# Kernel tuning notes

Measured on AMD Instinct MI355X. Metric: run time of the kernel, lower is better.

## Reference

```python
import jax, jax.numpy as jnp
import numpy as np

M_CH = 2        # channels == sources
K = 8           # NMF bases
N_ITER = 8
SWITCH_ITER = 5
ALPHA = 0.1
BETA = 0.0
EPS = 1e-10
I_BINS = 1025   # freq bins (n_fft=2048)
J_FRAMES = 4096 # STFT frames


def setup_inputs() -> dict:
    key = jax.random.key(0)
    ks = jax.random.split(key, 5)
    X = jax.random.normal(ks[0], (M_CH, J_FRAMES, I_BINS, 2), jnp.float32)
    T_s = jax.random.uniform(ks[1], (I_BINS, K), jnp.float32) * 0.1 + EPS
    V_s = jax.random.uniform(ks[2], (K, J_FRAMES), jnp.float32) * 0.1 + EPS
    T_n = jax.random.uniform(ks[3], (I_BINS, K), jnp.float32) * 0.1 + EPS
    V_n = jax.random.uniform(ks[4], (K, J_FRAMES), jnp.float32) * 0.1 + EPS
    return {"X": X, "T_s": T_s, "V_s": V_s, "T_n": T_n, "V_n": V_n}


def _ilrma_noisy(X, T_s, V_s, T_n, V_n):
    M, J, I, _ = X.shape
    eps, alpha, beta = EPS, ALPHA, BETA
    # (M,J,I,2) -> complex (I,M,J)
    Xc = (X[..., 0] + 1j * X[..., 1]).astype(jnp.complex64).transpose(2, 0, 1)
    eyeM = jnp.eye(M, dtype=jnp.complex64)
    W = jnp.broadcast_to(eyeM, (I, M, M))
    Y = jnp.einsum('inm,inj->imj', W.conj(), Xc)  # W^H X
    lam_n = jnp.ones((I,), jnp.float32)
    r_s = jnp.maximum(T_s @ V_s, eps)
    r_n = jnp.maximum(T_n @ V_n, eps)

    for it in range(N_ITER):
        if it < SWITCH_ITER:
            r_s = jnp.maximum(T_s @ V_s, eps)
            r_n = jnp.maximum(T_n @ V_n, eps)
        lam = lam_n[:, None]
        Lam = jnp.maximum(r_s + r_n * lam, eps)
        Y1 = Y[:, 0, :]
        p1 = jnp.abs(Y1) ** 2                          # (I,J)
        pn = jnp.sum(jnp.abs(Y[:, 1:, :]) ** 2, axis=1)  # (I,J)
        invL = 1.0 / Lam
        invL2 = invL * invL
        if it < SWITCH_ITER:
            # --- T_s ---
            T_s = jnp.maximum(T_s * jnp.sqrt(((p1 * invL2) @ V_s.T) / ((invL @ V_s.T) + eps)), eps)
            r_s = jnp.maximum(T_s @ V_s, eps)
            Lam = jnp.maximum(r_s + r_n * lam, eps); invL = 1.0 / Lam; invL2 = invL * invL
            # --- V_s ---
            V_s = jnp.maximum(V_s * jnp.sqrt((T_s.T @ (p1 * invL2)) / ((T_s.T @ invL) + eps)), eps)
            r_s = jnp.maximum(T_s @ V_s, eps)
            Lam = jnp.maximum(r_s + r_n * lam, eps); invL = 1.0 / Lam; invL2 = invL * invL
            inv_rn = 1.0 / r_n; inv_rn2 = inv_rn * inv_rn
            # --- T_n ---
            Tn_num = (lam * p1 * invL2) @ V_n.T + (pn * inv_rn2) @ V_n.T
            Tn_den = (lam * invL) @ V_n.T + (M - 1) * (inv_rn @ V_n.T) + eps
            T_n = jnp.maximum(T_n * jnp.sqrt(Tn_num / Tn_den), eps)
            r_n = jnp.maximum(T_n @ V_n, eps)
            Lam = jnp.maximum(r_s + r_n * lam, eps); invL = 1.0 / Lam; invL2 = invL * invL
            inv_rn = 1.0 / r_n; inv_rn2 = inv_rn * inv_rn
            # --- V_n ---
            Vn_num = T_n.T @ (lam * p1 * invL2) + T_n.T @ (pn * inv_rn2)
            Vn_den = T_n.T @ (lam * invL) + (M - 1) * (T_n.T @ inv_rn) + eps
            V_n = jnp.maximum(V_n * jnp.sqrt(Vn_num / Vn_den), eps)
            r_n = jnp.maximum(T_n @ V_n, eps)
            r_s = jnp.maximum(T_s @ V_s, eps)
            Lam = jnp.maximum(r_s + r_n * lam, eps); invL = 1.0 / Lam; invL2 = invL * invL
            # --- lambda_n ---
            lam_num = jnp.sum(r_n * p1 * invL2, axis=1)
            lam_den = jnp.sum(r_n * invL, axis=1) + eps
            lam_n = jnp.maximum(lam_n * jnp.sqrt(lam_num / lam_den), eps)
            Lam = jnp.maximum(r_s + r_n * lam_n[:, None], eps)
            # --- GEVD demixing update per frequency bin ---
            Xw_s = Xc * jnp.sqrt(1.0 / Lam)[:, None, :]
            Xw_n = Xc * jnp.sqrt(1.0 / r_n)[:, None, :]
            G_s = jnp.einsum('imj,inj->imn', Xw_s, Xw_s.conj()) / J + eps * eyeM
            G_n = jnp.einsum('imj,inj->imn', Xw_n, Xw_n.conj()) / J + eps * eyeM
            L = jnp.linalg.cholesky(G_s)
            Linv = jnp.linalg.inv(L)
            LinvH = jnp.conj(jnp.swapaxes(Linv, 1, 2))
            C = Linv @ G_n @ LinvH
            evals, evecs = jnp.linalg.eigh(C)  # ascending eigenvalues
            Vg = LinvH @ evecs                 # (I,M,M) generalized eigenvectors
            cols = []
            for m in range(M):
                h = Vg[:, :, m]                # (I,M); eigh already sorts ascending
                G = G_s if m == 0 else G_n
                quad = jnp.real(jnp.einsum('im,imn,in->i', h.conj(), G, h))
                cols.append(h / jnp.sqrt(jnp.maximum(quad, eps))[:, None])
            W = jnp.stack(cols, axis=2)
            Y = jnp.einsum('inm,inj->imj', W.conj(), Xc)
        else:
            # Phase 2: fix W, unconstrained r updates with inverse-gamma prior
            inv_rs = 1.0 / (r_s + eps); inv_rs2 = inv_rs * inv_rs
            inv_rn = 1.0 / (r_n + eps); inv_rn2 = inv_rn * inv_rn
            r_s = jnp.maximum(r_s * jnp.sqrt((p1 * invL2 + beta * inv_rs2) / (invL + (alpha + 1.0) * inv_rs + eps)), eps)
            Lam = jnp.maximum(r_s + r_n * lam, eps); invL = 1.0 / Lam; invL2 = invL * invL
            r_n = jnp.maximum(r_n * jnp.sqrt((lam * p1 * invL2 + pn * inv_rn2) / (lam * invL + (M - 1) * inv_rn + eps)), eps)
            Lam = jnp.maximum(r_s + r_n * lam, eps); invL = 1.0 / Lam; invL2 = invL * invL
            lam_num = jnp.sum(r_n * p1 * invL2, axis=1)
            lam_den = jnp.sum(r_n * invL, axis=1) + eps
            lam_n = jnp.maximum(lam_n * jnp.sqrt(lam_num / lam_den), eps)

    # Final single-channel Wiener extraction of the target, replicated over M
    Lam = jnp.maximum(r_s + r_n * lam_n[:, None], eps)
    S = (r_s / Lam) * Y[:, 0, :]                       # (I,J) complex
    S_ri = jnp.stack([jnp.real(S).T, jnp.imag(S).T], axis=-1)  # (J,I,2)
    return jnp.broadcast_to(S_ri[None], (M, J, I, 2)).astype(jnp.float32)


def reference(X, T_s, V_s, T_n, V_n):
    return _ilrma_noisy(X, T_s, V_s, T_n, V_n)
```

## Files before the change

kernel.cpp:

```cpp
#include <hip/hip_runtime.h>
#include <math.h>

#define IB 1025
#define JF 4096
#define EPSF 1e-10f

__device__ __forceinline__ void load8(const float* __restrict__ base, int i, float v[8]) {
  const float4* b4 = (const float4*)(base + i * 8);
  float4 a = b4[0], b = b4[1];
  v[0]=a.x; v[1]=a.y; v[2]=a.z; v[3]=a.w; v[4]=b.x; v[5]=b.y; v[6]=b.z; v[7]=b.w;
}
__device__ __forceinline__ float dot8(const float a[8], const float b[8]) {
  float s = a[0]*b[0];
#pragma unroll
  for (int k=1;k<8;k++) s += a[k]*b[k];
  return s;
}

__global__ __launch_bounds__(256) void k_init(
    const float* __restrict__ Ts_in, const float* __restrict__ Vs_in,
    const float* __restrict__ Tn_in, const float* __restrict__ Vn_in,
    float* __restrict__ Ts, float* __restrict__ Vs,
    float* __restrict__ Tn, float* __restrict__ Vn,
    float* __restrict__ lam, float* __restrict__ Wm) {
  int idx = blockIdx.x * 256 + threadIdx.x;
  if (idx < 8 * JF) { Vs[idx] = Vs_in[idx]; Vn[idx] = Vn_in[idx]; }
  if (idx < IB * 8) { Ts[idx] = Ts_in[idx]; Tn[idx] = Tn_in[idx]; }
  if (idx < IB) {
    lam[idx] = 1.0f;
    float* w = Wm + idx * 8;
    w[0]=1.f; w[1]=0.f; w[2]=0.f; w[3]=0.f; w[4]=0.f; w[5]=0.f; w[6]=1.f; w[7]=0.f;
  }
}

__global__ __launch_bounds__(1024) void k_p1pn_ts(const float2* __restrict__ X2,
    const float* __restrict__ Wm,
    const float* __restrict__ Ts, const float* __restrict__ Vs,
    const float* __restrict__ Tn, const float* __restrict__ Vn,
    const float* __restrict__ lam,
    float* __restrict__ p1, float* __restrict__ pn, float* __restrict__ P) {
  int tx = threadIdx.x, ty = threadIdx.y;
  int i = blockIdx.x * 256 + tx;
  int jc = blockIdx.y;
  bool ok = (i < IB);
  float ts[8], tn[8], lamv = 0.f;
  float4 wa = make_float4(0,0,0,0), wb = make_float4(0,0,0,0);
  if (ok) {
    load8(Ts, i, ts); load8(Tn, i, tn); lamv = lam[i];
    const float4* W4 = (const float4*)Wm;
    wa = W4[i*2]; wb = W4[i*2+1];
  }
  float num[8] = {0,0,0,0,0,0,0,0}, den[8] = {0,0,0,0,0,0,0,0};
  int j0 = jc * 16 + ty * 4;
  for (int jj = 0; jj < 4; jj++) {
    int j = j0 + jj;
    float vs[8], vn[8];
#pragma unroll
    for (int k=0;k<8;k++){ vs[k]=Vs[k*JF+j]; vn[k]=Vn[k*JF+j]; }
    if (ok) {
      float2 x0 = X2[j*IB + i];
      float2 x1 = X2[(JF + j)*IB + i];
      float y0r = wa.x*x0.x + wa.y*x0.y + wa.z*x1.x + wa.w*x1.y;
      float y0i = wa.x*x0.y - wa.y*x0.x + wa.z*x1.y - wa.w*x1.x;
      float y1r = wb.x*x0.x + wb.y*x0.y + wb.z*x1.x + wb.w*x1.y;
      float y1i = wb.x*x0.y - wb.y*x0.x + wb.z*x1.y - wb.w*x1.x;
      float pv  = y0r*y0r + y0i*y0i;
      float pnv = y1r*y1r + y1i*y1i;
      p1[j*IB + i] = pv;
      pn[j*IB + i] = pnv;
      float rs = fmaxf(dot8(ts, vs), EPSF);
      float rn = fmaxf(dot8(tn, vn), EPSF);
      float iL = 1.f / fmaxf(rs + rn*lamv, EPSF);
      float a2 = pv*iL*iL;
#pragma unroll
      for (int k=0;k<8;k++){ num[k] += a2*vs[k]; den[k] += iL*vs[k]; }
    }
  }
  __shared__ float red[16][4][256];
#pragma unroll
  for (int v=0;v<8;v++){ red[v][ty][tx] = num[v]; red[8+v][ty][tx] = den[v]; }
  __syncthreads();
  if (ok) {
#pragma unroll
    for (int u=0;u<4;u++){
      int v = ty*4+u;
      float s = red[v][0][tx]+red[v][1][tx]+red[v][2][tx]+red[v][3][tx];
      P[(jc*16+v)*IB + i] = s;
    }
  }
}

__global__ __launch_bounds__(512) void k_t_final(const float* __restrict__ P, float* __restrict__ T) {
  int tx = threadIdx.x;
  int ii = tx & 63, g = tx >> 6;
  int i = blockIdx.x * 64 + ii;
  int k = blockIdx.y;
  float num = 0.f, den = 0.f;
  if (i < IB) {
    for (int t = 0; t < 32; t++) {
      int c = g*32 + t;
      num += P[(c*16+k)*IB + i];
      den += P[(c*16+8+k)*IB + i];
    }
  }
  __shared__ float red[2][8][64];
  red[0][g][ii] = num; red[1][g][ii] = den;
  __syncthreads();
  if (g == 0 && i < IB) {
    float n_ = 0.f, d_ = 0.f;
#pragma unroll
    for (int q=0;q<8;q++){ n_ += red[0][q][ii]; d_ += red[1][q][ii]; }
    float t = T[i*8+k];
    T[i*8+k] = fmaxf(t * sqrtf(n_/(d_+EPSF)), EPSF);
  }
}

__global__ __launch_bounds__(256) void k_vs(const float* __restrict__ p1,
    const float* __restrict__ Ts, float* __restrict__ Vs,
    const float* __restrict__ Tn, const float* __restrict__ Vn,
    const float* __restrict__ lam) {
  int j = blockIdx.x;
  int tx = threadIdx.x;
  float vs[8], vn[8];
#pragma unroll
  for (int k=0;k<8;k++){ vs[k]=Vs[k*JF+j]; vn[k]=Vn[k*JF+j]; }
  float acc[16];
#pragma unroll
  for (int v=0;v<16;v++) acc[v] = 0.f;
  for (int s = 0; s < 5; s++) {
    int i = s*256 + tx;
    if (i < IB) {
      float ts[8], tn[8];
      load8(Ts, i, ts); load8(Tn, i, tn);
      float lamv = lam[i];
      float pv = p1[j*IB + i];
      float rs = fmaxf(dot8(ts, vs), EPSF);
      float rn = fmaxf(dot8(tn, vn), EPSF);
      float iL = 1.f / fmaxf(rs + rn*lamv, EPSF);
      float a2 = pv*iL*iL;
#pragma unroll
      for (int k=0;k<8;k++){ acc[k] += ts[k]*a2; acc[8+k] += ts[k]*iL; }
    }
  }
  __shared__ float red[4][16];
  int wid = tx >> 6, lane = tx & 63;
#pragma unroll
  for (int v=0;v<16;v++){
    float x = acc[v];
    x += __shfl_down(x, 32, 64); x += __shfl_down(x, 16, 64);
    x += __shfl_down(x, 8, 64);  x += __shfl_down(x, 4, 64);
    x += __shfl_down(x, 2, 64);  x += __shfl_down(x, 1, 64);
    if (lane == 0) red[wid][v] = x;
  }
  __syncthreads();
  if (tx == 0) {
#pragma unroll
    for (int k=0;k<8;k++){
      float n_ = red[0][k]+red[1][k]+red[2][k]+red[3][k];
      float d_ = red[0][8+k]+red[1][8+k]+red[2][8+k]+red[3][8+k];
      Vs[k*JF+j] = fmaxf(vs[k] * sqrtf(n_/(d_+EPSF)), EPSF);
    }
  }
}

__global__ __launch_bounds__(1024) void k_tn_partial(const float* __restrict__ p1,
    const float* __restrict__ pn,
    const float* __restrict__ Ts, const float* __restrict__ Vs,
    const float* __restrict__ Tn, const float* __restrict__ Vn,
    const float* __restrict__ lam, float* __restrict__ P) {
  int tx = threadIdx.x, ty = threadIdx.y;
  int i = blockIdx.x * 256 + tx;
  int jc = blockIdx.y;
  bool ok = (i < IB);
  float ts[8], tn[8], lamv = 0.f;
  if (ok) { load8(Ts, i, ts); load8(Tn, i, tn); lamv = lam[i]; }
  float num[8] = {0,0,0,0,0,0,0,0}, den[8] = {0,0,0,0,0,0,0,0};
  int j0 = jc * 16 + ty * 4;
  for (int jj = 0; jj < 4; jj++) {
    int j = j0 + jj;
    float vs[8], vn[8];
#pragma unroll
    for (int k=0;k<8;k++){ vs[k]=Vs[k*JF+j]; vn[k]=Vn[k*JF+j]; }
    if (ok) {
      float pv = p1[j*IB + i];
      float pnv = pn[j*IB + i];
      float rs = fmaxf(dot8(ts, vs), EPSF);
      float rn = fmaxf(dot8(tn, vn), EPSF);
      float iL = 1.f / fmaxf(rs + rn*lamv, EPSF);
      float irn = 1.f / rn;
      float a2 = lamv*pv*iL*iL + pnv*irn*irn;
      float b2 = lamv*iL + irn;
#pragma unroll
      for (int k=0;k<8;k++){ num[k] += a2*vn[k]; den[k] += b2*vn[k]; }
    }
  }
  __shared__ float red[16][4][256];
#pragma unroll
  for (int v=0;v<8;v++){ red[v][ty][tx] = num[v]; red[8+v][ty][tx] = den[v]; }
  __syncthreads();
  if (ok) {
#pragma unroll
    for (int u=0;u<4;u++){
      int v = ty*4+u;
      float s = red[v][0][tx]+red[v][1][tx]+red[v][2][tx]+red[v][3][tx];
      P[(jc*16+v)*IB + i] = s;
    }
  }
}

__global__ __launch_bounds__(256) void k_vn(const float* __restrict__ p1,
    const float* __restrict__ pn,
    const float* __restrict__ Ts, const float* __restrict__ Vs,
    const float* __restrict__ Tn, float* __restrict__ Vn,
    const float* __restrict__ lam) {
  int j = blockIdx.x;
  int tx = threadIdx.x;
  float vs[8], vn[8];
#pragma unroll
  for (int k=0;k<8;k++){ vs[k]=Vs[k*JF+j]; vn[k]=Vn[k*JF+j]; }
  float acc[16];
#pragma unroll
  for (int v=0;v<16;v++) acc[v] = 0.f;
  for (int s = 0; s < 5; s++) {
    int i = s*256 + tx;
    if (i < IB) {
      float ts[8], tn[8];
      load8(Ts, i, ts); load8(Tn, i, tn);
      float lamv = lam[i];
      float pv = p1[j*IB + i];
      float pnv = pn[j*IB + i];
      float rs = fmaxf(dot8(ts, vs), EPSF);
      float rn = fmaxf(dot8(tn, vn), EPSF);
      float iL = 1.f / fmaxf(rs + rn*lamv, EPSF);
      float irn = 1.f / rn;
      float a2 = lamv*pv*iL*iL + pnv*irn*irn;
      float b2 = lamv*iL + irn;
#pragma unroll
      for (int k=0;k<8;k++){ acc[k] += tn[k]*a2; acc[8+k] += tn[k]*b2; }
    }
  }
  __shared__ float red[4][16];
  int wid = tx >> 6, lane = tx & 63;
#pragma unroll
  for (int v=0;v<16;v++){
    float x = acc[v];
    x += __shfl_down(x, 32, 64); x += __shfl_down(x, 16, 64);
    x += __shfl_down(x, 8, 64);  x += __shfl_down(x, 4, 64);
    x += __shfl_down(x, 2, 64);  x += __shfl_down(x, 1, 64);
    if (lane == 0) red[wid][v] = x;
  }
  __syncthreads();
  if (tx == 0) {
#pragma unroll
    for (int k=0;k<8;k++){
      float n_ = red[0][k]+red[1][k]+red[2][k]+red[3][k];
      float d_ = red[0][8+k]+red[1][8+k]+red[2][8+k]+red[3][8+k];
      Vn[k*JF+j] = fmaxf(vn[k] * sqrtf(n_/(d_+EPSF)), EPSF);
    }
  }
}

__global__ __launch_bounds__(1024) void k_lam_partial(const float* __restrict__ p1,
    const float* __restrict__ Ts, const float* __restrict__ Vs,
    const float* __restrict__ Tn, const float* __restrict__ Vn,
    const float* __restrict__ lam, float* __restrict__ P) {
  int tx = threadIdx.x, ty = threadIdx.y;
  int i = blockIdx.x * 256 + tx;
  int jc = blockIdx.y;
  bool ok = (i < IB);
  float ts[8], tn[8], lamv = 0.f;
  if (ok) { load8(Ts, i, ts); load8(Tn, i, tn); lamv = lam[i]; }
  float lnum = 0.f, lden = 0.f;
  int j0 = jc * 16 + ty * 4;
  for (int jj = 0; jj < 4; jj++) {
    int j = j0 + jj;
    float vs[8], vn[8];
#pragma unroll
    for (int k=0;k<8;k++){ vs[k]=Vs[k*JF+j]; vn[k]=Vn[k*JF+j]; }
    if (ok) {
      float pv = p1[j*IB + i];
      float rs = fmaxf(dot8(ts, vs), EPSF);
      float rn = fmaxf(dot8(tn, vn), EPSF);
      float iL = 1.f / fmaxf(rs + rn*lamv, EPSF);
      lnum += rn*pv*iL*iL;
      lden += rn*iL;
    }
  }
  __shared__ float red[2][4][256];
  red[0][ty][tx] = lnum; red[1][ty][tx] = lden;
  __syncthreads();
  if (ty < 2 && ok) {
    float s = red[ty][0][tx]+red[ty][1][tx]+red[ty][2][tx]+red[ty][3][tx];
    P[(jc*2+ty)*IB + i] = s;
  }
}

__global__ __launch_bounds__(512) void k_lam_final(const float* __restrict__ P, float* __restrict__ lam,
                                                   int nchunks) {
  int tx = threadIdx.x;
  int ii = tx & 63, g = tx >> 6;
  int i = blockIdx.x * 64 + ii;
  int per = nchunks >> 3;
  float num = 0.f, den = 0.f;
  if (i < IB) {
    for (int t = 0; t < per; t++) {
      int c = g*per + t;
      num += P[(c*2+0)*IB + i];
      den += P[(c*2+1)*IB + i];
    }
  }
  __shared__ float red[2][8][64];
  red[0][g][ii] = num; red[1][g][ii] = den;
  __syncthreads();
  if (g == 0 && i < IB) {
    float n_ = 0.f, d_ = 0.f;
#pragma unroll
    for (int q=0;q<8;q++){ n_ += red[0][q][ii]; d_ += red[1][q][ii]; }
    lam[i] = fmaxf(lam[i] * sqrtf(n_/(d_+EPSF)), EPSF);
  }
}

__global__ __launch_bounds__(1024) void k_g_partial(const float2* __restrict__ X2,
    const float* __restrict__ Ts, const float* __restrict__ Vs,
    const float* __restrict__ Tn, const float* __restrict__ Vn,
    const float* __restrict__ lam, float* __restrict__ P) {
  int tx = threadIdx.x, ty = threadIdx.y;
  int i = blockIdx.x * 256 + tx;
  int jc = blockIdx.y;
  bool ok = (i < IB);
  float ts[8], tn[8], lamv = 0.f;
  if (ok) { load8(Ts, i, ts); load8(Tn, i, tn); lamv = lam[i]; }
  float g[8];
#pragma unroll
  for (int v=0;v<8;v++) g[v] = 0.f;
  int j0 = jc * 16 + ty * 4;
  for (int jj = 0; jj < 4; jj++) {
    int j = j0 + jj;
    float vs[8], vn[8];
#pragma unroll
    for (int k=0;k<8;k++){ vs[k]=Vs[k*JF+j]; vn[k]=Vn[k*JF+j]; }
    if (ok) {
      float2 x0 = X2[j*IB + i];
      float2 x1 = X2[(JF + j)*IB + i];
      float rs = fmaxf(dot8(ts, vs), EPSF);
      float rn = fmaxf(dot8(tn, vn), EPSF);
      float ws = 1.f / fmaxf(rs + rn*lamv, EPSF);
      float wn = 1.f / rn;
      float m00 = x0.x*x0.x + x0.y*x0.y;
      float m11 = x1.x*x1.x + x1.y*x1.y;
      float m01r = x0.x*x1.x + x0.y*x1.y;
      float m01i = x0.y*x1.x - x0.x*x1.y;
      g[0] += m00*ws; g[1] += m11*ws; g[2] += m01r*ws; g[3] += m01i*ws;
      g[4] += m00*wn; g[5] += m11*wn; g[6] += m01r*wn; g[7] += m01i*wn;
    }
  }
  __shared__ float red[8][4][256];
#pragma unroll
  for (int v=0;v<8;v++) red[v][ty][tx] = g[v];
  __syncthreads();
  if (ok) {
#pragma unroll
    for (int u=0;u<2;u++){
      int v = ty*2+u;
      float s = red[v][0][tx]+red[v][1][tx]+red[v][2][tx]+red[v][3][tx];
      P[(jc*8+v)*IB + i] = s;
    }
  }
}

__global__ __launch_bounds__(512) void k_g_final(const float* __restrict__ P, double* __restrict__ Gd) {
  int tx = threadIdx.x;
  int ii = tx & 63, g = tx >> 6;
  int i = blockIdx.x * 64 + ii;
  int v = blockIdx.y;
  double s = 0.0;
  if (i < IB) {
    for (int t = 0; t < 32; t++) {
      int c = g*32 + t;
      s += (double)P[(c*8+v)*IB + i];
    }
  }
  __shared__ double red[8][64];
  red[g][ii] = s;
  __syncthreads();
  if (g == 0 && i < IB) {
    double acc = 0.0;
#pragma unroll
    for (int q=0;q<8;q++) acc += red[q][ii];
    Gd[v*1028 + i] = acc;
  }
}

__device__ void dlaev2_dev(double a, double b, double c,
                           double& rt1, double& rt2, double& cs1, double& sn1) {
  double sm = a + c, df = a - c;
  double adf = fabs(df);
  double tb = b + b;
  double ab = fabs(tb);
  double acmx, acmn;
  if (fabs(a) > fabs(c)) { acmx = a; acmn = c; } else { acmx = c; acmn = a; }
  double rt;
  if (adf > ab)      { double t = ab/adf; rt = adf*sqrt(1.0 + t*t); }
  else if (adf < ab) { double t = adf/ab; rt = ab*sqrt(1.0 + t*t); }
  else               rt = ab*sqrt(2.0);
  int sgn1;
  if (sm < 0.0)      { rt1 = 0.5*(sm - rt); sgn1 = -1; rt2 = (acmx/rt1)*acmn - (b/rt1)*b; }
  else if (sm > 0.0) { rt1 = 0.5*(sm + rt); sgn1 =  1; rt2 = (acmx/rt1)*acmn - (b/rt1)*b; }
  else               { rt1 = 0.5*rt; rt2 = -0.5*rt; sgn1 = 1; }
  double cs; int sgn2;
  if (df >= 0.0) { cs = df + rt; sgn2 = 1; } else { cs = df - rt; sgn2 = -1; }
  double acs = fabs(cs);
  if (acs > ab) {
    double ct = -tb/cs;
    sn1 = 1.0/sqrt(1.0 + ct*ct);
    cs1 = ct*sn1;
  } else {
    if (ab == 0.0) { cs1 = 1.0; sn1 = 0.0; }
    else { double tn = -cs/tb; cs1 = 1.0/sqrt(1.0 + tn*tn); sn1 = tn*cs1; }
  }
  if (sgn1 == sgn2) { double tn = cs1; cs1 = -sn1; sn1 = tn; }
}

__global__ __launch_bounds__(64) void k_eig(const double* __restrict__ Gd, float* __restrict__ Wm) {
  int i = blockIdx.x * 64 + threadIdx.x;
  if (i >= IB) return;
  double g[8];
#pragma unroll
  for (int v=0;v<8;v++) g[v] = Gd[v*1028 + i];
  const double EPSD = 1e-10;
  double as  = g[0]/4096.0 + EPSD;
  double cs_ = g[1]/4096.0 + EPSD;
  double bsr = g[2]/4096.0, bsi = g[3]/4096.0;
  double dn  = g[4]/4096.0 + EPSD;
  double fn  = g[5]/4096.0 + EPSD;
  double enr = g[6]/4096.0, eni = g[7]/4096.0;
  double l11 = sqrt(as);
  double il11 = 1.0/l11;
  double l21r = bsr*il11, l21i = -bsi*il11;
  double l22sq = cs_ - (l21r*l21r + l21i*l21i);
  double l22 = sqrt(fmax(l22sq, 0.0));
  double p = il11, r = 1.0/l22;
  double qr = -l21r*p*r, qi = -l21i*p*r;
  double C00  = p*p*dn;
  double C01r = p*(dn*qr + enr*r);
  double C01i = p*(-dn*qi + eni*r);
  double C11  = (qr*qr+qi*qi)*dn + 2.0*r*(qr*enr - qi*eni) + r*r*fn;
  double br = C01r, bi = C01i;
  double e_, hqr, hqi;
  if (bi == 0.0) { e_ = br; hqr = 1.0; hqi = 0.0; }
  else {
    double ab_ = sqrt(br*br + bi*bi);
    e_ = (br >= 0.0) ? -ab_ : ab_;
    hqr = br / e_; hqi = -bi / e_;
  }
  double ut0, ub0, ut1, ub1;
  const double MEPS = 1.1102230246251565e-16;
  if (fabs(e_) <= sqrt(fabs(C00))*sqrt(fabs(C11))*MEPS) {
    if (C11 < C00) { ut0=0.0; ub0=1.0; ut1=1.0; ub1=0.0; }
    else           { ut0=1.0; ub0=0.0; ut1=0.0; ub1=1.0; }
  } else {
    double rt1, rt2, cs1, sn1;
    dlaev2_dev(C00, e_, C11, rt1, rt2, cs1, sn1);
    if (rt2 < rt1) { ut0=-sn1; ub0=cs1; ut1=cs1;  ub1=sn1; }
    else           { ut0=cs1;  ub0=sn1; ut1=-sn1; ub1=cs1; }
  }
  double chr = qr*hqr + qi*hqi;
  double chi = qr*hqi - qi*hqr;
  double v0tr = p*ut0 + chr*ub0, v0ti = chi*ub0;
  double v0br = r*hqr*ub0,       v0bi = r*hqi*ub0;
  double v1tr = p*ut1 + chr*ub1, v1ti = chi*ub1;
  double v1br = r*hqr*ub1,       v1bi = r*hqi*ub1;
  double q0 = as*(v0tr*v0tr+v0ti*v0ti) + cs_*(v0br*v0br+v0bi*v0bi)
            + 2.0*((bsr*v0br - bsi*v0bi)*v0tr + (bsr*v0bi + bsi*v0br)*v0ti);
  double q1 = dn*(v1tr*v1tr+v1ti*v1ti) + fn*(v1br*v1br+v1bi*v1bi)
            + 2.0*((enr*v1br - eni*v1bi)*v1tr + (enr*v1bi + eni*v1br)*v1ti);
  double s0 = 1.0/sqrt(fmax(q0, 1e-10));
  double s1 = 1.0/sqrt(fmax(q1, 1e-10));
  float* w = Wm + i*8;
  w[0] = (float)(v0tr*s0); w[1] = (float)(v0ti*s0);
  w[2] = (float)(v0br*s0); w[3] = (float)(v0bi*s0);
  w[4] = (float)(v1tr*s1); w[5] = (float)(v1ti*s1);
  w[6] = (float)(v1br*s1); w[7] = (float)(v1bi*s1);
}

__global__ __launch_bounds__(256) void k_p1pn_rinit(const float2* __restrict__ X2,
    const float* __restrict__ Wm,
    const float* __restrict__ Ts, const float* __restrict__ Vs,
    const float* __restrict__ Tn, const float* __restrict__ Vn,
    float* __restrict__ p1, float* __restrict__ pn, float2* __restrict__ m0) {
  int i = blockIdx.x * 256 + threadIdx.x;
  int j = blockIdx.y;
  if (i >= IB) return;
  float2 x0 = X2[j*IB + i];
  float2 x1 = X2[(JF + j)*IB + i];
  const float4* W4 = (const float4*)Wm;
  float4 wa = W4[i*2], wb = W4[i*2+1];
  float y0r = wa.x*x0.x + wa.y*x0.y + wa.z*x1.x + wa.w*x1.y;
  float y0i = wa.x*x0.y - wa.y*x0.x + wa.z*x1.y - wa.w*x1.x;
  float y1r = wb.x*x0.x + wb.y*x0.y + wb.z*x1.x + wb.w*x1.y;
  float y1i = wb.x*x0.y - wb.y*x0.x + wb.z*x1.y - wb.w*x1.x;
  p1[j*IB + i] = y0r*y0r + y0i*y0i;
  pn[j*IB + i] = y1r*y1r + y1i*y1i;
  float ts[8], tn[8];
  load8(Ts, i, ts); load8(Tn, i, tn);
  float rs = 0.f, rn = 0.f;
#pragma unroll
  for (int k=0;k<8;k++){ rs += ts[k]*Vs[k*JF+j]; rn += tn[k]*Vn[k*JF+j]; }
  m0[j*IB + i] = make_float2(fmaxf(rs, EPSF), fmaxf(rn, EPSF));
}

__global__ __launch_bounds__(1024) void k_simp(float2* __restrict__ m0,
    const float* __restrict__ p1, const float* __restrict__ pn,
    const float* __restrict__ lam, float* __restrict__ P) {
  int tx = threadIdx.x, ty = threadIdx.y;
  int i = blockIdx.x * 256 + tx;
  int jc = blockIdx.y;
  bool ok = (i < IB);
  float lamv = ok ? lam[i] : 0.f;
  float lnum = 0.f, lden = 0.f;
  int j0 = jc * 32 + ty * 8;
  for (int jj = 0; jj < 8; jj++) {
    int j = j0 + jj;
    if (ok) {
      float2 rr = m0[j*IB + i];
      float rs = rr.x, rn = rr.y;
      float pv = p1[j*IB + i], pnv = pn[j*IB + i];
      float iL = 1.f / fmaxf(rs + rn*lamv, EPSF);
      float irs = 1.f / (rs + EPSF);
      float rs2 = fmaxf(rs * sqrtf((pv*iL*iL) / (iL + 1.1f*irs + EPSF)), EPSF);
      float iL2 = 1.f / fmaxf(rs2 + rn*lamv, EPSF);
      float irn = 1.f / (rn + EPSF);
      float rn2 = fmaxf(rn * sqrtf((lamv*pv*iL2*iL2 + pnv*irn*irn) / (lamv*iL2 + irn + EPSF)), EPSF);
      float iL3 = 1.f / fmaxf(rs2 + rn2*lamv, EPSF);
      m0[j*IB + i] = make_float2(rs2, rn2);
      lnum += rn2*pv*iL3*iL3;
      lden += rn2*iL3;
    }
  }
  __shared__ float red[2][4][256];
  red[0][ty][tx] = lnum; red[1][ty][tx] = lden;
  __syncthreads();
  if (ty < 2 && ok) {
    float s = red[ty][0][tx]+red[ty][1][tx]+red[ty][2][tx]+red[ty][3][tx];
    P[(jc*2+ty)*IB + i] = s;
  }
}

__global__ __launch_bounds__(256) void k_final(float2* __restrict__ m0, float2* __restrict__ m1,
    const float2* __restrict__ X2, const float* __restrict__ Wm, const float* __restrict__ lam) {
  int i = blockIdx.x * 256 + threadIdx.x;
  int j = blockIdx.y;
  if (i >= IB) return;
  float2 rr = m0[j*IB + i];
  float L = fmaxf(rr.x + rr.y*lam[i], EPSF);
  float gsc = rr.x / L;
  float2 x0 = X2[j*IB + i];
  float2 x1 = X2[(JF + j)*IB + i];
  float4 wa = ((const float4*)Wm)[i*2];
  float y0r = wa.x*x0.x + wa.y*x0.y + wa.z*x1.x + wa.w*x1.y;
  float y0i = wa.x*x0.y - wa.y*x0.x + wa.z*x1.y - wa.w*x1.x;
  float2 s = make_float2(gsc*y0r, gsc*y0i);
  m0[j*IB + i] = s;
  m1[j*IB + i] = s;
}

extern "C" void kernel_launch(void* const* d_in, const int* in_sizes, int n_in,
                              void* d_out, int out_size, void* d_ws, size_t ws_size,
                              hipStream_t stream) {
  (void)in_sizes; (void)n_in; (void)out_size; (void)ws_size;
  const float* X = (const float*)d_in[0];
  const float* Ts_in = (const float*)d_in[1];
  const float* Vs_in = (const float*)d_in[2];
  const float* Tn_in = (const float*)d_in[3];
  const float* Vn_in = (const float*)d_in[4];

  float* w = (float*)d_ws;
  float* Pt  = w;
  double* Gd = (double*)(w + 1049600);
  float* Ts  = w + 1049600 + 16448;
  float* Vs  = Ts + 8200;
  float* Tn  = Vs + 32768;
  float* Vn  = Tn + 8200;
  float* lam = Vn + 32768;
  float* Wm  = lam + 1028;

  float* out = (float*)d_out;
  float2* m0 = (float2*)d_out;
  float2* m1 = m0 + (size_t)JF*IB;
  float* p1 = out + 2*(size_t)JF*IB;
  float* pn = p1 + (size_t)JF*IB;
  float* Pbig = out;
  const float2* X2 = (const float2*)X;

  k_init<<<dim3(128), 256, 0, stream>>>(Ts_in, Vs_in, Tn_in, Vn_in, Ts, Vs, Tn, Vn, lam, Wm);

  for (int it = 0; it < 5; it++) {
    k_p1pn_ts<<<dim3(5, 256), dim3(256,4), 0, stream>>>(X2, Wm, Ts, Vs, Tn, Vn, lam, p1, pn, Pbig);
    k_t_final<<<dim3(17, 8), 512, 0, stream>>>(Pbig, Ts);
    k_vs<<<dim3(JF), 256, 0, stream>>>(p1, Ts, Vs, Tn, Vn, lam);
    k_tn_partial<<<dim3(5, 256), dim3(256,4), 0, stream>>>(p1, pn, Ts, Vs, Tn, Vn, lam, Pbig);
    k_t_final<<<dim3(17, 8), 512, 0, stream>>>(Pbig, Tn);
    k_vn<<<dim3(JF), 256, 0, stream>>>(p1, pn, Ts, Vs, Tn, Vn, lam);
    k_lam_partial<<<dim3(5, 256), dim3(256,4), 0, stream>>>(p1, Ts, Vs, Tn, Vn, lam, Pbig);
    k_lam_final<<<dim3(17), 512, 0, stream>>>(Pbig, lam, 256);
    k_g_partial<<<dim3(5, 256), dim3(256,4), 0, stream>>>(X2, Ts, Vs, Tn, Vn, lam, Pbig);
    k_g_final<<<dim3(17, 8), 512, 0, stream>>>(Pbig, Gd);
    k_eig<<<dim3(17), 64, 0, stream>>>(Gd, Wm);
  }

  k_p1pn_rinit<<<dim3(5, JF), 256, 0, stream>>>(X2, Wm, Ts, Vs, Tn, Vn, p1, pn, m0);

  for (int it = 0; it < 3; it++) {
    k_simp<<<dim3(5, 128), dim3(256,4), 0, stream>>>(m0, p1, pn, lam, Pt);
    k_lam_final<<<dim3(17), 512, 0, stream>>>(Pt, lam, 128);
  }

  k_final<<<dim3(5, JF), 256, 0, stream>>>(m0, m1, X2, Wm, lam);
}
```

Measured before the change: 1.043 ms.

## Stage V columns in shared memory and drop intra-block j reduction in partial kernels

The partial-reduction kernels now use 256-thread blocks, each thread handling 16 frames serially. The 16x8 V slices are staged once into shared memory instead of every thread re-reading them from global memory. The shared-memory cross-ty reduction and its barrier are removed, and partials are written directly. k_simp now uses 256 chunks of 16 frames to match, which doubles the partials k_lam_final has to reduce. Blocks get smaller with longer serial loops, so there are fewer waves per block and less latency hiding per thread.

```diff
diff --git a/kernel.cpp b/kernel.cpp
--- a/kernel.cpp
+++ b/kernel.cpp
@@ -11,6 +11,12 @@
   v[0]=a.x; v[1]=a.y; v[2]=a.z; v[3]=a.w; v[4]=b.x; v[5]=b.y; v[6]=b.z; v[7]=b.w;
 }
 __device__ __forceinline__ float dot8(const float a[8], const float b[8]) {
+  float s = a[0]*b[0];
+#pragma unroll
+  for (int k=1;k<8;k++) s += a[k]*b[k];
+  return s;
+}
+__device__ __forceinline__ float dot8s(const float a[8], const float* __restrict__ b) {
   float s = a[0]*b[0];
 #pragma unroll
   for (int k=1;k<8;k++) s += a[k]*b[k];
@@ -33,60 +39,58 @@
   }
 }
 
-__global__ __launch_bounds__(1024) void k_p1pn_ts(const float2* __restrict__ X2,
+#define STAGE_V(vsh, vnh, Vs, Vn, j0) do {                                  \
+    int t_ = threadIdx.x;                                                   \
+    if (t_ < 128) { int jj_ = t_ >> 3, k_ = t_ & 7;                         \
+      vsh[jj_][k_] = Vs[k_*JF + (j0) + jj_]; }                              \
+    else { int u_ = t_ - 128; int jj_ = u_ >> 3, k_ = u_ & 7;               \
+      vnh[jj_][k_] = Vn[k_*JF + (j0) + jj_]; }                              \
+    __syncthreads();                                                        \
+  } while (0)
+
+__global__ __launch_bounds__(256) void k_p1pn_ts(const float2* __restrict__ X2,
     const float* __restrict__ Wm,
     const float* __restrict__ Ts, const float* __restrict__ Vs,
     const float* __restrict__ Tn, const float* __restrict__ Vn,
     const float* __restrict__ lam,
     float* __restrict__ p1, float* __restrict__ pn, float* __restrict__ P) {
-  int tx = threadIdx.x, ty = threadIdx.y;
+  __shared__ float vsh[16][8], vnh[16][8];
+  int tx = threadIdx.x;
   int i = blockIdx.x * 256 + tx;
   int jc = blockIdx.y;
-  bool ok = (i < IB);
-  float ts[8], tn[8], lamv = 0.f;
-  float4 wa = make_float4(0,0,0,0), wb = make_float4(0,0,0,0);
-  if (ok) {
-    load8(Ts, i, ts); load8(Tn, i, tn); lamv = lam[i];
-    const float4* W4 = (const float4*)Wm;
-    wa = W4[i*2]; wb = W4[i*2+1];
-  }
+  int j0 = jc * 16;
+  STAGE_V(vsh, vnh, Vs, Vn, j0);
+  if (i >= IB) return;
+  float ts[8], tn[8];
+  load8(Ts, i, ts); load8(Tn, i, tn);
+  float lamv = lam[i];
+  const float4* W4 = (const float4*)Wm;
+  float4 wa = W4[i*2], wb = W4[i*2+1];
   float num[8] = {0,0,0,0,0,0,0,0}, den[8] = {0,0,0,0,0,0,0,0};
-  int j0 = jc * 16 + ty * 4;
-  for (int jj = 0; jj < 4; jj++) {
+#pragma unroll 4
+  for (int jj = 0; jj < 16; jj++) {
     int j = j0 + jj;
-    float vs[8], vn[8];
-#pragma unroll
-    for (int k=0;k<8;k++){ vs[k]=Vs[k*JF+j]; vn[k]=Vn[k*JF+j]; }
-    if (ok) {
-      float2 x0 = X2[j*IB + i];
-      float2 x1 = X2[(JF + j)*IB + i];
-      float y0r = wa.x*x0.x + wa.y*x0.y + wa.z*x1.x + wa.w*x1.y;
-      float y0i = wa.x*x0.y - wa.y*x0.x + wa.z*x1.y - wa.w*x1.x;
-      float y1r = wb.x*x0.x + wb.y*x0.y + wb.z*x1.x + wb.w*x1.y;
-      float y1i = wb.x*x0.y - wb.y*x0.x + wb.z*x1.y - wb.w*x1.x;
-      float pv  = y0r*y0r + y0i*y0i;
-      float pnv = y1r*y1r + y1i*y1i;
-      p1[j*IB + i] = pv;
-      pn[j*IB + i] = pnv;
-      float rs = fmaxf(dot8(ts, vs), EPSF);
-      float rn = fmaxf(dot8(tn, vn), EPSF);
-      float iL = 1.f / fmaxf(rs + rn*lamv, EPSF);
-      float a2 = pv*iL*iL;
-#pragma unroll
-      for (int k=0;k<8;k++){ num[k] += a2*vs[k]; den[k] += iL*vs[k]; }
-    }
-  }
-  __shared__ float red[16][4][256];
-#pragma unroll
-  for (int v=0;v<8;v++){ red[v][ty][tx] = num[v]; red[8+v][ty][tx] = den[v]; }
-  __syncthreads();
-  if (ok) {
-#pragma unroll
-    for (int u=0;u<4;u++){
-      int v = ty*4+u;
-      float s = red[v][0][tx]+red[v][1][tx]+red[v][2][tx]+red[v][3][tx];
-      P[(jc*16+v)*IB + i] = s;
-    }
+    float2 x0 = X2[j*IB + i];
+    float2 x1 = X2[(JF + j)*IB + i];
+    float y0r = wa.x*x0.x + wa.y*x0.y + wa.z*x1.x + wa.w*x1.y;
+    float y0i = wa.x*x0.y - wa.y*x0.x + wa.z*x1.y - wa.w*x1.x;
+    float y1r = wb.x*x0.x + wb.y*x0.y + wb.z*x1.x + wb.w*x1.y;
+    float y1i = wb.x*x0.y - wb.y*x0.x + wb.z*x1.y - wb.w*x1.x;
+    float pv  = y0r*y0r + y0i*y0i;
+    float pnv = y1r*y1r + y1i*y1i;
+    p1[j*IB + i] = pv;
+    pn[j*IB + i] = pnv;
+    float rs = fmaxf(dot8s(ts, vsh[jj]), EPSF);
+    float rn = fmaxf(dot8s(tn, vnh[jj]), EPSF);
+    float iL = 1.f / fmaxf(rs + rn*lamv, EPSF);
+    float a2 = pv*iL*iL;
+#pragma unroll
+    for (int k=0;k<8;k++){ num[k] += a2*vsh[jj][k]; den[k] += iL*vsh[jj][k]; }
+  }
+#pragma unroll
+  for (int k=0;k<8;k++){
+    P[(jc*16+k)*IB + i] = num[k];
+    P[(jc*16+8+k)*IB + i] = den[k];
   }
 }
 
@@ -163,48 +167,40 @@
   }
 }
 
-__global__ __launch_bounds__(1024) void k_tn_partial(const float* __restrict__ p1,
+__global__ __launch_bounds__(256) void k_tn_partial(const float* __restrict__ p1,
     const float* __restrict__ pn,
     const float* __restrict__ Ts, const float* __restrict__ Vs,
     const float* __restrict__ Tn, const float* __restrict__ Vn,
     const float* __restrict__ lam, float* __restrict__ P) {
-  int tx = threadIdx.x, ty = threadIdx.y;
+  __shared__ float vsh[16][8], vnh[16][8];
+  int tx = threadIdx.x;
   int i = blockIdx.x * 256 + tx;
   int jc = blockIdx.y;
-  bool ok = (i < IB);
-  float ts[8], tn[8], lamv = 0.f;
-  if (ok) { load8(Ts, i, ts); load8(Tn, i, tn); lamv = lam[i]; }
+  int j0 = jc * 16;
+  STAGE_V(vsh, vnh, Vs, Vn, j0);
+  if (i >= IB) return;
+  float ts[8], tn[8];
+  load8(Ts, i, ts); load8(Tn, i, tn);
+  float lamv = lam[i];
   float num[8] = {0,0,0,0,0,0,0,0}, den[8] = {0,0,0,0,0,0,0,0};
-  int j0 = jc * 16 + ty * 4;
-  for (int jj = 0; jj < 4; jj++) {
+#pragma unroll 4
+  for (int jj = 0; jj < 16; jj++) {
     int j = j0 + jj;
-    float vs[8], vn[8];
-#pragma unroll
-    for (int k=0;k<8;k++){ vs[k]=Vs[k*JF+j]; vn[k]=Vn[k*JF+j]; }
-    if (ok) {
-      float pv = p1[j*IB + i];
-      float pnv = pn[j*IB + i];
-      float rs = fmaxf(dot8(ts, vs), EPSF);
-      float rn = fmaxf(dot8(tn, vn), EPSF);
-      float iL = 1.f / fmaxf(rs + rn*lamv, EPSF);
-      float irn = 1.f / rn;
-      float a2 = lamv*pv*iL*iL + pnv*irn*irn;
-      float b2 = lamv*iL + irn;
-#pragma unroll
-      for (int k=0;k<8;k++){ num[k] += a2*vn[k]; den[k] += b2*vn[k]; }
-    }
-  }
-  __shared__ float red[16][4][256];
-#pragma unroll
-  for (int v=0;v<8;v++){ red[v][ty][tx] = num[v]; red[8+v][ty][tx] = den[v]; }
-  __syncthreads();
-  if (ok) {
-#pragma unroll
-    for (int u=0;u<4;u++){
-      int v = ty*4+u;
-      float s = red[v][0][tx]+red[v][1][tx]+red[v][2][tx]+red[v][3][tx];
-      P[(jc*16+v)*IB + i] = s;
-    }
+    float pv = p1[j*IB + i];
+    float pnv = pn[j*IB + i];
+    float rs = fmaxf(dot8s(ts, vsh[jj]), EPSF);
+    float rn = fmaxf(dot8s(tn, vnh[jj]), EPSF);
+    float iL = 1.f / fmaxf(rs + rn*lamv, EPSF);
+    float irn = 1.f / rn;
+    float a2 = lamv*pv*iL*iL + pnv*irn*irn;
+    float b2 = lamv*iL + irn;
+#pragma unroll
+    for (int k=0;k<8;k++){ num[k] += a2*vnh[jj][k]; den[k] += b2*vnh[jj][k]; }
+  }
+#pragma unroll
+  for (int k=0;k<8;k++){
+    P[(jc*16+k)*IB + i] = num[k];
+    P[(jc*16+8+k)*IB + i] = den[k];
   }
 }
 
@@ -260,39 +256,33 @@
   }
 }
 
-__global__ __launch_bounds__(1024) void k_lam_partial(const float* __restrict__ p1,
+__global__ __launch_bounds__(256) void k_lam_partial(const float* __restrict__ p1,
     const float* __restrict__ Ts, const float* __restrict__ Vs,
     const float* __restrict__ Tn, const float* __restrict__ Vn,
     const float* __restrict__ lam, float* __restrict__ P) {
-  int tx = threadIdx.x, ty = threadIdx.y;
+  __shared__ float vsh[16][8], vnh[16][8];
+  int tx = threadIdx.x;
   int i = blockIdx.x * 256 + tx;
   int jc = blockIdx.y;
-  bool ok = (i < IB);
-  float ts[8], tn[8], lamv = 0.f;
-  if (ok) { load8(Ts, i, ts); load8(Tn, i, tn); lamv = lam[i]; }
+  int j0 = jc * 16;
+  STAGE_V(vsh, vnh, Vs, Vn, j0);
+  if (i >= IB) return;
+  float ts[8], tn[8];
+  load8(Ts, i, ts); load8(Tn, i, tn);
+  float lamv = lam[i];
   float lnum = 0.f, lden = 0.f;
-  int j0 = jc * 16 + ty * 4;
-  for (int jj = 0; jj < 4; jj++) {
+#pragma unroll 4
+  for (int jj = 0; jj < 16; jj++) {
     int j = j0 + jj;
-    float vs[8], vn[8];
-#pragma unroll
-    for (int k=0;k<8;k++){ vs[k]=Vs[k*JF+j]; vn[k]=Vn[k*JF+j]; }
-    if (ok) {
-      float pv = p1[j*IB + i];
-      float rs = fmaxf(dot8(ts, vs), EPSF);
-      float rn = fmaxf(dot8(tn, vn), EPSF);
-      float iL = 1.f / fmaxf(rs + rn*lamv, EPSF);
-      lnum += rn*pv*iL*iL;
-      lden += rn*iL;
-    }
-  }
-  __shared__ float red[2][4][256];
-  red[0][ty][tx] = lnum; red[1][ty][tx] = lden;
-  __syncthreads();
-  if (ty < 2 && ok) {
-    float s = red[ty][0][tx]+red[ty][1][tx]+red[ty][2][tx]+red[ty][3][tx];
-    P[(jc*2+ty)*IB + i] = s;
-  }
+    float pv = p1[j*IB + i];
+    float rs = fmaxf(dot8s(ts, vsh[jj]), EPSF);
+    float rn = fmaxf(dot8s(tn, vnh[jj]), EPSF);
+    float iL = 1.f / fmaxf(rs + rn*lamv, EPSF);
+    lnum += rn*pv*iL*iL;
+    lden += rn*iL;
+  }
+  P[(jc*2+0)*IB + i] = lnum;
+  P[(jc*2+1)*IB + i] = lden;
 }
 
 __global__ __launch_bounds__(512) void k_lam_final(const float* __restrict__ P, float* __restrict__ lam,
@@ -320,52 +310,41 @@
   }
 }
 
-__global__ __launch_bounds__(1024) void k_g_partial(const float2* __restrict__ X2,
+__global__ __launch_bounds__(256) void k_g_partial(const float2* __restrict__ X2,
     const float* __restrict__ Ts, const float* __restrict__ Vs,
     const float* __restrict__ Tn, const float* __restrict__ Vn,
     const float* __restrict__ lam, float* __restrict__ P) {
-  int tx = threadIdx.x, ty = threadIdx.y;
+  __shared__ float vsh[16][8], vnh[16][8];
+  int tx = threadIdx.x;
   int i = blockIdx.x * 256 + tx;
   int jc = blockIdx.y;
-  bool ok = (i < IB);
-  float ts[8], tn[8], lamv = 0.f;
-  if (ok) { load8(Ts, i, ts); load8(Tn, i, tn); lamv = lam[i]; }
+  int j0 = jc * 16;
+  STAGE_V(vsh, vnh, Vs, Vn, j0);
+  if (i >= IB) return;
+  float ts[8], tn[8];
+  load8(Ts, i, ts); load8(Tn, i, tn);
+  float lamv = lam[i];
   float g[8];
 #pragma unroll
   for (int v=0;v<8;v++) g[v] = 0.f;
-  int j0 = jc * 16 + ty * 4;
-  for (int jj = 0; jj < 4; jj++) {
+#pragma unroll 4
+  for (int jj = 0; jj < 16; jj++) {
     int j = j0 + jj;
-    float vs[8], vn[8];
-#pragma unroll
-    for (int k=0;k<8;k++){ vs[k]=Vs[k*JF+j]; vn[k]=Vn[k*JF+j]; }
-    if (ok) {
-      float2 x0 = X2[j*IB + i];
-      float2 x1 = X2[(JF + j)*IB + i];
-      float rs = fmaxf(dot8(ts, vs), EPSF);
-      float rn = fmaxf(dot8(tn, vn), EPSF);
-      float ws = 1.f / fmaxf(rs + rn*lamv, EPSF);
-      float wn = 1.f / rn;
-      float m00 = x0.x*x0.x + x0.y*x0.y;
-      float m11 = x1.x*x1.x + x1.y*x1.y;
-      float m01r = x0.x*x1.x + x0.y*x1.y;
-      float m01i = x0.y*x1.x - x0.x*x1.y;
-      g[0] += m00*ws; g[1] += m11*ws; g[2] += m01r*ws; g[3] += m01i*ws;
-      g[4] += m00*wn; g[5] += m11*wn; g[6] += m01r*wn; g[7] += m01i*wn;
-    }
-  }
-  __shared__ float red[8][4][256];
-#pragma unroll
-  for (int v=0;v<8;v++) red[v][ty][tx] = g[v];
-  __syncthreads();
-  if (ok) {
-#pragma unroll
-    for (int u=0;u<2;u++){
-      int v = ty*2+u;
-      float s = red[v][0][tx]+red[v][1][tx]+red[v][2][tx]+red[v][3][tx];
-      P[(jc*8+v)*IB + i] = s;
-    }
-  }
+    float2 x0 = X2[j*IB + i];
+    float2 x1 = X2[(JF + j)*IB + i];
+    float rs = fmaxf(dot8s(ts, vsh[jj]), EPSF);
+    float rn = fmaxf(dot8s(tn, vnh[jj]), EPSF);
+    float ws = 1.f / fmaxf(rs + rn*lamv, EPSF);
+    float wn = 1.f / rn;
+    float m00 = x0.x*x0.x + x0.y*x0.y;
+    float m11 = x1.x*x1.x + x1.y*x1.y;
+    float m01r = x0.x*x1.x + x0.y*x1.y;
+    float m01i = x0.y*x1.x - x0.x*x1.y;
+    g[0] += m00*ws; g[1] += m11*ws; g[2] += m01r*ws; g[3] += m01i*ws;
+    g[4] += m00*wn; g[5] += m11*wn; g[6] += m01r*wn; g[7] += m01i*wn;
+  }
+#pragma unroll
+  for (int v=0;v<8;v++) P[(jc*8+v)*IB + i] = g[v];
 }
 
 __global__ __launch_bounds__(512) void k_g_final(const float* __restrict__ P, double* __restrict__ Gd) {
@@ -509,41 +488,35 @@
   m0[j*IB + i] = make_float2(fmaxf(rs, EPSF), fmaxf(rn, EPSF));
 }
 
-__global__ __launch_bounds__(1024) void k_simp(float2* __restrict__ m0,
+__global__ __launch_bounds__(256) void k_simp(float2* __restrict__ m0,
     const float* __restrict__ p1, const float* __restrict__ pn,
     const float* __restrict__ lam, float* __restrict__ P) {
-  int tx = threadIdx.x, ty = threadIdx.y;
+  int tx = threadIdx.x;
   int i = blockIdx.x * 256 + tx;
   int jc = blockIdx.y;
-  bool ok = (i < IB);
-  float lamv = ok ? lam[i] : 0.f;
+  if (i >= IB) return;
+  float lamv = lam[i];
   float lnum = 0.f, lden = 0.f;
-  int j0 = jc * 32 + ty * 8;
-  for (int jj = 0; jj < 8; jj++) {
+  int j0 = jc * 16;
+#pragma unroll 4
+  for (int jj = 0; jj < 16; jj++) {
     int j = j0 + jj;
-    if (ok) {
-      float2 rr = m0[j*IB + i];
-      float rs = rr.x, rn = rr.y;
-      float pv = p1[j*IB + i], pnv = pn[j*IB + i];
-      float iL = 1.f / fmaxf(rs + rn*lamv, EPSF);
-      float irs = 1.f / (rs + EPSF);
-      float rs2 = fmaxf(rs * sqrtf((pv*iL*iL) / (iL + 1.1f*irs + EPSF)), EPSF);
-      float iL2 = 1.f / fmaxf(rs2 + rn*lamv, EPSF);
-      float irn = 1.f / (rn + EPSF);
-      float rn2 = fmaxf(rn * sqrtf((lamv*pv*iL2*iL2 + pnv*irn*irn) / (lamv*iL2 + irn + EPSF)), EPSF);
-      float iL3 = 1.f / fmaxf(rs2 + rn2*lamv, EPSF);
-      m0[j*IB + i] = make_float2(rs2, rn2);
-      lnum += rn2*pv*iL3*iL3;
-      lden += rn2*iL3;
-    }
-  }
-  __shared__ float red[2][4][256];
-  red[0][ty][tx] = lnum; red[1][ty][tx] = lden;
-  __syncthreads();
-  if (ty < 2 && ok) {
-    float s = red[ty][0][tx]+red[ty][1][tx]+red[ty][2][tx]+red[ty][3][tx];
-    P[(jc*2+ty)*IB + i] = s;
-  }
+    float2 rr = m0[j*IB + i];
+    float rs = rr.x, rn = rr.y;
+    float pv = p1[j*IB + i], pnv = pn[j*IB + i];
+    float iL = 1.f / fmaxf(rs + rn*lamv, EPSF);
+    float irs = 1.f / (rs + EPSF);
+    float rs2 = fmaxf(rs * sqrtf((pv*iL*iL) / (iL + 1.1f*irs + EPSF)), EPSF);
+    float iL2 = 1.f / fmaxf(rs2 + rn*lamv, EPSF);
+    float irn = 1.f / (rn + EPSF);
+    float rn2 = fmaxf(rn * sqrtf((lamv*pv*iL2*iL2 + pnv*irn*irn) / (lamv*iL2 + irn + EPSF)), EPSF);
+    float iL3 = 1.f / fmaxf(rs2 + rn2*lamv, EPSF);
+    m0[j*IB + i] = make_float2(rs2, rn2);
+    lnum += rn2*pv*iL3*iL3;
+    lden += rn2*iL3;
+  }
+  P[(jc*2+0)*IB + i] = lnum;
+  P[(jc*2+1)*IB + i] = lden;
 }
 
 __global__ __launch_bounds__(256) void k_final(float2* __restrict__ m0, float2* __restrict__ m1,
@@ -595,15 +568,15 @@
   k_init<<<dim3(128), 256, 0, stream>>>(Ts_in, Vs_in, Tn_in, Vn_in, Ts, Vs, Tn, Vn, lam, Wm);
 
   for (int it = 0; it < 5; it++) {
-    k_p1pn_ts<<<dim3(5, 256), dim3(256,4), 0, stream>>>(X2, Wm, Ts, Vs, Tn, Vn, lam, p1, pn, Pbig);
+    k_p1pn_ts<<<dim3(5, 256), 256, 0, stream>>>(X2, Wm, Ts, Vs, Tn, Vn, lam, p1, pn, Pbig);
     k_t_final<<<dim3(17, 8), 512, 0, stream>>>(Pbig, Ts);
     k_vs<<<dim3(JF), 256, 0, stream>>>(p1, Ts, Vs, Tn, Vn, lam);
-    k_tn_partial<<<dim3(5, 256), dim3(256,4), 0, stream>>>(p1, pn, Ts, Vs, Tn, Vn, lam, Pbig);
+    k_tn_partial<<<dim3(5, 256), 256, 0, stream>>>(p1, pn, Ts, Vs, Tn, Vn, lam, Pbig);
     k_t_final<<<dim3(17, 8), 512, 0, stream>>>(Pbig, Tn);
     k_vn<<<dim3(JF), 256, 0, stream>>>(p1, pn, Ts, Vs, Tn, Vn, lam);
-    k_lam_partial<<<dim3(5, 256), dim3(256,4), 0, stream>>>(p1, Ts, Vs, Tn, Vn, lam, Pbig);
+    k_lam_partial<<<dim3(5, 256), 256, 0, stream>>>(p1, Ts, Vs, Tn, Vn, lam, Pbig);
     k_lam_final<<<dim3(17), 512, 0, stream>>>(Pbig, lam, 256);
-    k_g_partial<<<dim3(5, 256), dim3(256,4), 0, stream>>>(X2, Ts, Vs, Tn, Vn, lam, Pbig);
+    k_g_partial<<<dim3(5, 256), 256, 0, stream>>>(X2, Ts, Vs, Tn, Vn, lam, Pbig);
     k_g_final<<<dim3(17, 8), 512, 0, stream>>>(Pbig, Gd);
     k_eig<<<dim3(17), 64, 0, stream>>>(Gd, Wm);
   }
@@ -611,8 +584,8 @@
   k_p1pn_rinit<<<dim3(5, JF), 256, 0, stream>>>(X2, Wm, Ts, Vs, Tn, Vn, p1, pn, m0);
 
   for (int it = 0; it < 3; it++) {
-    k_simp<<<dim3(5, 128), dim3(256,4), 0, stream>>>(m0, p1, pn, lam, Pt);
-    k_lam_final<<<dim3(17), 512, 0, stream>>>(Pt, lam, 128);
+    k_simp<<<dim3(5, 256), 256, 0, stream>>>(m0, p1, pn, lam, Pt);
+    k_lam_final<<<dim3(17), 512, 0, stream>>>(Pt, lam, 256);
   }
 
   k_final<<<dim3(5, JF), 256, 0, stream>>>(m0, m1, X2, Wm, lam);
```

After: 872.3 us. 16.3% less time.
